# Kernel tuning notes

Hardware: AMD Instinct MI355X
Metric: run time of the kernel (lower is better)

The kernel has to match this reference:

```python
import jax, jax.numpy as jnp
import numpy as np

HEADS = 4
DIM_HEAD = 32
GROUPS = 32  # min(256//4, 32)
EPS = 1e-5


def setup_inputs() -> dict:
    key = jax.random.key(0)
    ks = jax.random.split(key, 5)
    B, C, H, W = 16, 256, 64, 64
    CD, HC, WC = 512, 32, 32
    hid = HEADS * DIM_HEAD  # 128
    return {
        "x": jax.random.normal(ks[0], (B, C, H, W), jnp.float32),
        "cond": jax.random.normal(ks[1], (B, CD, HC, WC), jnp.float32),
        "gn_w": jnp.ones((C,), jnp.float32),
        "gn_b": jnp.zeros((C,), jnp.float32),
        "w_q": jax.random.normal(ks[2], (hid, C), jnp.float32) * 0.05,
        "b_q": jnp.zeros((hid,), jnp.float32),
        "w_kv": jax.random.normal(ks[3], (2 * hid, CD), jnp.float32) * 0.05,
        "b_kv": jnp.zeros((2 * hid,), jnp.float32),
        "w_out": jax.random.normal(ks[4], (C, hid), jnp.float32) * 0.05,
        "b_out": jnp.zeros((C,), jnp.float32),
    }


def _group_norm(x, w, b):
    # x: (B, C, H, W); normalize per group over (channels-in-group, H, W)
    B, C, H, W = x.shape
    xg = x.reshape(B, GROUPS, C // GROUPS, H, W)
    mu = jnp.mean(xg, axis=(2, 3, 4), keepdims=True)
    var = jnp.var(xg, axis=(2, 3, 4), keepdims=True)
    xn = ((xg - mu) * jax.lax.rsqrt(var + EPS)).reshape(B, C, H, W)
    return xn * w[None, :, None, None] + b[None, :, None, None]


def _conv1x1(x, w, b):
    # x: (B, Cin, H, W), w: (Cout, Cin), b: (Cout,)
    return jnp.einsum('oc,bchw->bohw', w, x) + b[None, :, None, None]


def reference(x, cond, gn_w, gn_b, w_q, b_q, w_kv, b_kv, w_out, b_out):
    B, C, H, W = x.shape
    hid = HEADS * DIM_HEAD
    xn = _group_norm(x, gn_w, gn_b)
    q = _conv1x1(xn, w_q, b_q)          # (B, hid, H, W)
    kv = _conv1x1(cond, w_kv, b_kv)     # (B, 2*hid, Hc, Wc)
    Nc = kv.shape[2] * kv.shape[3]
    N = H * W
    k = kv[:, :hid].reshape(B, HEADS, DIM_HEAD, Nc)
    v = kv[:, hid:].reshape(B, HEADS, DIM_HEAD, Nc)
    q = q.reshape(B, HEADS, DIM_HEAD, N)
    k = jax.nn.softmax(k, axis=-1)
    # kv outer product: (B, heads, d, e)
    context = jnp.einsum('bhdn,bhen->bhde', k, v)
    # query contraction over d: (B, heads, e, n)
    out = jnp.einsum('bhde,bhdn->bhen', context, q)
    out = out.reshape(B, hid, H, W)
    return _conv1x1(out, w_out, b_out)
```

## Files before the change

kernel.cpp:

```cpp
#include <hip/hip_runtime.h>
#include <hip/hip_bf16.h>

typedef __attribute__((ext_vector_type(8))) short bf16x8;
typedef __attribute__((ext_vector_type(4))) float f32x4;

__device__ __forceinline__ ushort f2bf(float f) {
    __hip_bfloat16 h = __float2bfloat16(f);
    return __builtin_bit_cast(ushort, h);
}
__device__ __forceinline__ float bflo(unsigned u) { return __uint_as_float(u << 16); }
__device__ __forceinline__ float bfhi(unsigned u) { return __uint_as_float(u & 0xffff0000u); }

__device__ __forceinline__ void unpack8(uint4 r, float* o) {
    o[0] = bflo(r.x); o[1] = bfhi(r.x); o[2] = bflo(r.y); o[3] = bfhi(r.y);
    o[4] = bflo(r.z); o[5] = bfhi(r.z); o[6] = bflo(r.w); o[7] = bfhi(r.w);
}

__global__ void cvtw_kernel(const float* __restrict__ w, ushort* __restrict__ o,
                            float* __restrict__ zbase) {
    int i = blockIdx.x * 256 + threadIdx.x;
    if (i < 68608) zbase[i] = 0.f;
    o[i] = f2bf(w[i]);
}

__global__ __launch_bounds__(256) void kvstats_kernel(const ushort* __restrict__ wkv16,
                                                      const float* __restrict__ cond,
                                                      const float* __restrict__ b_kv,
                                                      ushort* __restrict__ kv16,
                                                      const float* __restrict__ x,
                                                      float* __restrict__ statacc) {
    __shared__ ushort lA[64 * 64];
    __shared__ ushort lB[64 * 64];
    __shared__ float scratch[64 * 64];
    __shared__ float red[8];
    int bid = blockIdx.x;
    int t = threadIdx.x;
    if (bid < 1024) {
        int nb = bid & 15, ob = (bid >> 4) & 3, b = bid >> 6;
        int col0 = nb * 64, row0 = ob * 64;
        int l = t & 63, wid = t >> 6;
        int wr = wid >> 1, wc = wid & 1;
        int lr = l & 15, lg = l >> 4;
        const ushort* Ab = wkv16 + (size_t)row0 * 512;
        const float* Bb = cond + (size_t)b * 512 * 1024 + col0;
        int sp = t & 31, sj = t >> 5;
        uint4 a0_, a1_;
        float4 b0_, b1_, b2_, b3_;
        int rA0 = t >> 3,        gA0 = (t & 7) ^ (rA0 & 7);
        int rA1 = 32 + (t >> 3), gA1 = (t & 7) ^ (rA1 & 7);
        int rB = t >> 4, gB = t & 15;
#define KV_LOADA(k0) { \
        a0_ = *(const uint4*)(Ab + (size_t)rA0 * 512 + (k0) + gA0 * 8); \
        a1_ = *(const uint4*)(Ab + (size_t)rA1 * 512 + (k0) + gA1 * 8); }
#define KV_LOADB(k0) { \
        b0_ = *(const float4*)&Bb[(size_t)((k0) + rB)      * 1024 + gB * 4]; \
        b1_ = *(const float4*)&Bb[(size_t)((k0) + 16 + rB) * 1024 + gB * 4]; \
        b2_ = *(const float4*)&Bb[(size_t)((k0) + 32 + rB) * 1024 + gB * 4]; \
        b3_ = *(const float4*)&Bb[(size_t)((k0) + 48 + rB) * 1024 + gB * 4]; }
        KV_LOADA(0); KV_LOADB(0);
        f32x4 acc00 = {}, acc01 = {}, acc10 = {}, acc11 = {};
        for (int it = 0; it < 8; ++it) {
            *(uint4*)((char*)lA + (size_t)t * 16) = a0_;
            *(uint4*)((char*)lA + (size_t)(256 + t) * 16) = a1_;
            *(float4*)((char*)scratch + (rB)      * 256 + (gB ^ (((rB)      >> 1) & 15)) * 16) = b0_;
            *(float4*)((char*)scratch + (16 + rB) * 256 + (gB ^ (((16 + rB) >> 1) & 15)) * 16) = b1_;
            *(float4*)((char*)scratch + (32 + rB) * 256 + (gB ^ (((32 + rB) >> 1) & 15)) * 16) = b2_;
            *(float4*)((char*)scratch + (48 + rB) * 256 + (gB ^ (((48 + rB) >> 1) & 15)) * 16) = b3_;
            __syncthreads();
            if (it < 7) { KV_LOADA(it * 64 + 64); KV_LOADB(it * 64 + 64); }
            {
                int swz = sp & 15;
                float4 s0 = *(const float4*)((char*)scratch + (2*sp)   * 256 + ((2*sj)   ^ swz) * 16);
                float4 s1 = *(const float4*)((char*)scratch + (2*sp)   * 256 + ((2*sj+1) ^ swz) * 16);
                float4 s2 = *(const float4*)((char*)scratch + (2*sp+1) * 256 + ((2*sj)   ^ swz) * 16);
                float4 s3 = *(const float4*)((char*)scratch + (2*sp+1) * 256 + ((2*sj+1) ^ swz) * 16);
                float c0v[8] = {s0.x, s0.y, s0.z, s0.w, s1.x, s1.y, s1.z, s1.w};
                float c1v[8] = {s2.x, s2.y, s2.z, s2.w, s3.x, s3.y, s3.z, s3.w};
                #pragma unroll
                for (int w = 0; w < 8; ++w) {
                    int n = sj * 8 + w;
                    unsigned pk = (unsigned)f2bf(c0v[w]) | ((unsigned)f2bf(c1v[w]) << 16);
                    *(unsigned*)((char*)lB + n * 128 + (((sp >> 2) ^ (n & 7)) * 16) + (sp & 3) * 4) = pk;
                }
            }
            __syncthreads();
            #pragma unroll
            for (int ks = 0; ks < 2; ++ks) {
                bf16x8 av0, av1, bv0, bv1;
                {
                    int ar = wr * 32 + lr, q = (ks * 4 + lg) ^ (ar & 7);
                    av0 = *(const bf16x8*)((const char*)lA + ar * 128 + q * 16);
                }
                {
                    int ar = wr * 32 + 16 + lr, q = (ks * 4 + lg) ^ (ar & 7);
                    av1 = *(const bf16x8*)((const char*)lA + ar * 128 + q * 16);
                }
                {
                    int br = wc * 32 + lr, q = (ks * 4 + lg) ^ (br & 7);
                    bv0 = *(const bf16x8*)((const char*)lB + br * 128 + q * 16);
                }
                {
                    int br = wc * 32 + 16 + lr, q = (ks * 4 + lg) ^ (br & 7);
                    bv1 = *(const bf16x8*)((const char*)lB + br * 128 + q * 16);
                }
                acc00 = __builtin_amdgcn_mfma_f32_16x16x32_bf16(av0, bv0, acc00, 0, 0, 0);
                acc01 = __builtin_amdgcn_mfma_f32_16x16x32_bf16(av0, bv1, acc01, 0, 0, 0);
                acc10 = __builtin_amdgcn_mfma_f32_16x16x32_bf16(av1, bv0, acc10, 0, 0, 0);
                acc11 = __builtin_amdgcn_mfma_f32_16x16x32_bf16(av1, bv1, acc11, 0, 0, 0);
            }
            __syncthreads();
        }
#undef KV_LOADA
#undef KV_LOADB
        int orow = row0 + wr * 32, ocol = col0 + wc * 32 + lr;
        #pragma unroll
        for (int mi = 0; mi < 2; ++mi) {
            int rb = orow + mi * 16 + lg * 4;
            float4 b4 = *(const float4*)&b_kv[rb];
            float bvr[4] = {b4.x, b4.y, b4.z, b4.w};
            f32x4 aacc0 = mi == 0 ? acc00 : acc10;
            f32x4 aacc1 = mi == 0 ? acc01 : acc11;
            #pragma unroll
            for (int r = 0; r < 4; ++r) {
                kv16[((size_t)b * 256 + rb + r) * 1024 + ocol]      = f2bf(aacc0[r] + bvr[r]);
                kv16[((size_t)b * 256 + rb + r) * 1024 + ocol + 16] = f2bf(aacc1[r] + bvr[r]);
            }
        }
    } else {
        int sid = bid - 1024;
        int bg = sid >> 2, q = sid & 3;
        const float4* xp = (const float4*)(x + (size_t)bg * 32768 + q * 8192);
        float s = 0.f, ss = 0.f;
        #pragma unroll
        for (int j = 0; j < 8; ++j) {
            float4 v = xp[t + 256 * j];
            s  += v.x + v.y + v.z + v.w;
            ss += v.x*v.x + v.y*v.y + v.z*v.z + v.w*v.w;
        }
        #pragma unroll
        for (int off = 32; off > 0; off >>= 1) {
            s  += __shfl_down(s, off, 64);
            ss += __shfl_down(ss, off, 64);
        }
        int wave = t >> 6;
        if ((t & 63) == 0) { red[wave * 2] = s; red[wave * 2 + 1] = ss; }
        __syncthreads();
        if (t == 0) {
            float S  = red[0] + red[2] + red[4] + red[6];
            float SS = red[1] + red[3] + red[5] + red[7];
            atomicAdd(&statacc[bg * 2],     S);
            atomicAdd(&statacc[bg * 2 + 1], SS);
        }
    }
}

__global__ __launch_bounds__(256) void ctx_partial_kernel(const ushort* __restrict__ kv,
                                                          float* __restrict__ rowsum,
                                                          float* __restrict__ ctx) {
    int bh = blockIdx.y, b = bh >> 2, h = bh & 3;
    int n0 = blockIdx.x * 128;
    __shared__ float pl[32][129], vl[32][129];
    int t = threadIdx.x;
    int r = t >> 3, cs = (t & 7) * 16;
    const ushort* kp = kv + ((size_t)b * 256 + h * 32 + r) * 1024 + n0 + cs;
    const ushort* vp = kv + ((size_t)b * 256 + 128 + h * 32 + r) * 1024 + n0 + cs;
    float kvals[16], vvals[16];
    unpack8(((const uint4*)kp)[0], kvals);
    unpack8(((const uint4*)kp)[1], kvals + 8);
    unpack8(((const uint4*)vp)[0], vvals);
    unpack8(((const uint4*)vp)[1], vvals + 8);
    float psum = 0.f;
    #pragma unroll
    for (int i = 0; i < 16; ++i) {
        float e = __expf(kvals[i]);
        pl[r][cs + i] = e;
        vl[r][cs + i] = vvals[i];
        psum += e;
    }
    psum += __shfl_xor(psum, 1, 64);
    psum += __shfl_xor(psum, 2, 64);
    psum += __shfl_xor(psum, 4, 64);
    if ((t & 7) == 0) atomicAdd(&rowsum[bh * 32 + r], psum);
    __syncthreads();
    int d0 = t >> 5, e0 = t & 31;
    float acc[4] = {0.f, 0.f, 0.f, 0.f};
    #pragma unroll 8
    for (int nn = 0; nn < 128; ++nn) {
        float vv = vl[e0][nn];
        #pragma unroll
        for (int i = 0; i < 4; ++i)
            acc[i] += pl[d0 + 8 * i][nn] * vv;
    }
    #pragma unroll
    for (int i = 0; i < 4; ++i)
        atomicAdd(&ctx[((size_t)bh * 32 + d0 + 8 * i) * 32 + e0], acc[i]);
}

__global__ __launch_bounds__(256) void a_kernel(const float* __restrict__ ctx,
                                                const float* __restrict__ rowsum,
                                                const float* __restrict__ w_out,
                                                const float* __restrict__ w_q,
                                                const float* __restrict__ b_q,
                                                const float* __restrict__ statacc,
                                                const float* __restrict__ gn_w,
                                                const float* __restrict__ gn_b,
                                                const float* __restrict__ b_out,
                                                ushort* __restrict__ A16,
                                                float* __restrict__ biasb) {
    __shared__ float ctxl[4][32][33];
    __shared__ float wol[16][128];
    __shared__ float ml[16][128];
    __shared__ float cbuf[256][17];
    __shared__ float pbuf[16][17];
    int b = blockIdx.x >> 4, ot = (blockIdx.x & 15) << 4;
    int t = threadIdx.x;
    #pragma unroll
    for (int j = 0; j < 16; ++j) {
        int e = t + 256 * j;
        float inv = 1.f / rowsum[b * 128 + (e >> 5)];
        ctxl[e >> 10][(e >> 5) & 31][e & 31] = ctx[(size_t)b * 4096 + e] * inv;
    }
    #pragma unroll
    for (int j = 0; j < 8; ++j) {
        int e = t + 256 * j;
        wol[e >> 7][e & 127] = w_out[(ot + (e >> 7)) * 128 + (e & 127)];
    }
    __syncthreads();
    #pragma unroll
    for (int j = 0; j < 8; ++j) {
        int e = t + 256 * j;
        int o = e >> 7, hd = e & 127, h = hd >> 5, d = hd & 31;
        float acc = 0.f;
        #pragma unroll
        for (int ee = 0; ee < 32; ++ee) acc += wol[o][h * 32 + ee] * ctxl[h][d][ee];
        ml[o][hd] = acc;
    }
    __syncthreads();
    int c = t, g = c >> 3;
    float a0 = statacc[(b * 32 + g) * 2], a1 = statacc[(b * 32 + g) * 2 + 1];
    float mu  = a0 * (1.f / 32768.f);
    float var = a1 * (1.f / 32768.f) - mu * mu;
    float sc = rsqrtf(var + 1e-5f) * gn_w[c];
    float tc = gn_b[c] - mu * sc;
    float wt[16];
    #pragma unroll
    for (int o = 0; o < 16; ++o) wt[o] = 0.f;
    for (int hd = 0; hd < 128; ++hd) {
        float wq = w_q[hd * 256 + c];
        #pragma unroll
        for (int o = 0; o < 16; ++o) wt[o] += ml[o][hd] * wq;
    }
    ushort* Abp = A16 + ((size_t)b * 256 + ot) * 256 + c;
    #pragma unroll
    for (int o = 0; o < 16; ++o) {
        Abp[(size_t)o * 256] = f2bf(wt[o] * sc);
        cbuf[c][o] = wt[o] * tc;
    }
    __syncthreads();
    {
        int o = t >> 4, seg = t & 15;
        float p = 0.f;
        #pragma unroll
        for (int i = 0; i < 16; ++i) p += cbuf[seg * 16 + i][o];
        pbuf[o][seg] = p;
    }
    __syncthreads();
    if (t < 16) {
        int o = t;
        float sum = 0.f;
        #pragma unroll
        for (int s2 = 0; s2 < 16; ++s2) sum += pbuf[o][s2];
        float md = 0.f;
        #pragma unroll 8
        for (int hd = 0; hd < 128; ++hd) md += ml[o][hd] * b_q[hd];
        biasb[(size_t)b * 256 + ot + o] = sum + md + b_out[ot + o];
    }
}

__global__ __launch_bounds__(512) void out_gemm_fused(const ushort* __restrict__ A16,
                                                      const float* __restrict__ x,
                                                      const float* __restrict__ biasb,
                                                      float* __restrict__ out) {
    __shared__ ushort lA[256 * 64];
    __shared__ ushort lB[128 * 64];
    __shared__ float scratch[64 * 128];
    int b = blockIdx.y;
    int n0 = blockIdx.x * 128;
    int t = threadIdx.x;
    int l = t & 63, wid = t >> 6;
    int wr = wid >> 1, wc = wid & 1;
    int lr = l & 15, lg = l >> 4;
    const ushort* Ab = A16 + (size_t)b * 65536;
    const float* xb = x + (size_t)b * 256 * 4096 + n0;
    int sp = t & 31, sj = t >> 5;
    uint4 a0_, a1_, a2_, a3_;
    float4 b0_, b1_, b2_, b3_;
    int rA = t >> 3, gA = (t & 7) ^ (rA & 7);
    int rB = t >> 5, gB = t & 31;
#define OG_LOADA(k0) { \
    a0_ = *(const uint4*)(Ab + (size_t)(rA)       * 256 + (k0) + gA * 8); \
    a1_ = *(const uint4*)(Ab + (size_t)(64 + rA)  * 256 + (k0) + gA * 8); \
    a2_ = *(const uint4*)(Ab + (size_t)(128 + rA) * 256 + (k0) + gA * 8); \
    a3_ = *(const uint4*)(Ab + (size_t)(192 + rA) * 256 + (k0) + gA * 8); }
#define OG_LOADB(k0) { \
    b0_ = *(const float4*)&xb[(size_t)((k0) + rB)      * 4096 + gB * 4]; \
    b1_ = *(const float4*)&xb[(size_t)((k0) + 16 + rB) * 4096 + gB * 4]; \
    b2_ = *(const float4*)&xb[(size_t)((k0) + 32 + rB) * 4096 + gB * 4]; \
    b3_ = *(const float4*)&xb[(size_t)((k0) + 48 + rB) * 4096 + gB * 4]; }
    OG_LOADA(0); OG_LOADB(0);
    f32x4 acc[4][4] = {};
    for (int it = 0; it < 4; ++it) {
        *(uint4*)((char*)lA + (size_t)t * 16)          = a0_;
        *(uint4*)((char*)lA + (size_t)(512 + t) * 16)  = a1_;
        *(uint4*)((char*)lA + (size_t)(1024 + t) * 16) = a2_;
        *(uint4*)((char*)lA + (size_t)(1536 + t) * 16) = a3_;
        *(float4*)((char*)scratch + (rB)      * 512 + (gB ^ (((rB)      >> 1) & 31)) * 16) = b0_;
        *(float4*)((char*)scratch + (16 + rB) * 512 + (gB ^ (((16 + rB) >> 1) & 31)) * 16) = b1_;
        *(float4*)((char*)scratch + (32 + rB) * 512 + (gB ^ (((32 + rB) >> 1) & 31)) * 16) = b2_;
        *(float4*)((char*)scratch + (48 + rB) * 512 + (gB ^ (((48 + rB) >> 1) & 31)) * 16) = b3_;
        __syncthreads();
        if (it < 3) { OG_LOADA(it * 64 + 64); OG_LOADB(it * 64 + 64); }
        {
            int swz = sp & 31;
            float4 s0 = *(const float4*)((char*)scratch + (2*sp)   * 512 + ((2*sj)   ^ swz) * 16);
            float4 s1 = *(const float4*)((char*)scratch + (2*sp)   * 512 + ((2*sj+1) ^ swz) * 16);
            float4 s2 = *(const float4*)((char*)scratch + (2*sp+1) * 512 + ((2*sj)   ^ swz) * 16);
            float4 s3 = *(const float4*)((char*)scratch + (2*sp+1) * 512 + ((2*sj+1) ^ swz) * 16);
            float c0v[8] = {s0.x, s0.y, s0.z, s0.w, s1.x, s1.y, s1.z, s1.w};
            float c1v[8] = {s2.x, s2.y, s2.z, s2.w, s3.x, s3.y, s3.z, s3.w};
            #pragma unroll
            for (int w = 0; w < 8; ++w) {
                int n = sj * 8 + w;
                unsigned pk = (unsigned)f2bf(c0v[w]) | ((unsigned)f2bf(c1v[w]) << 16);
                *(unsigned*)((char*)lB + n * 128 + (((sp >> 2) ^ (n & 7)) * 16) + (sp & 3) * 4) = pk;
            }
        }
        __syncthreads();
        #pragma unroll
        for (int ks = 0; ks < 2; ++ks) {
            bf16x8 av[4], bv[4];
            #pragma unroll
            for (int mi = 0; mi < 4; ++mi) {
                int ar = wr * 64 + mi * 16 + lr;
                int q = (ks * 4 + lg) ^ (ar & 7);
                av[mi] = *(const bf16x8*)((const char*)lA + ar * 128 + q * 16);
            }
            #pragma unroll
            for (int ni = 0; ni < 4; ++ni) {
                int br = wc * 64 + ni * 16 + lr;
                int q = (ks * 4 + lg) ^ (br & 7);
                bv[ni] = *(const bf16x8*)((const char*)lB + br * 128 + q * 16);
            }
            #pragma unroll
            for (int mi = 0; mi < 4; ++mi)
                #pragma unroll
                for (int ni = 0; ni < 4; ++ni)
                    acc[mi][ni] = __builtin_amdgcn_mfma_f32_16x16x32_bf16(
                        av[mi], bv[ni], acc[mi][ni], 0, 0, 0);
        }
        __syncthreads();
    }
#undef OG_LOADA
#undef OG_LOADB
    const float* bp = biasb + (size_t)b * 256;
    int orow = wr * 64, ocol = n0 + wc * 64 + lr;
    #pragma unroll
    for (int mi = 0; mi < 4; ++mi) {
        int rb = orow + mi * 16 + lg * 4;
        float4 b4 = *(const float4*)&bp[rb];
        float bvr[4] = {b4.x, b4.y, b4.z, b4.w};
        #pragma unroll
        for (int ni = 0; ni < 4; ++ni) {
            int cc = ocol + ni * 16;
            #pragma unroll
            for (int r = 0; r < 4; ++r)
                out[((size_t)b * 256 + rb + r) * 4096 + cc] = acc[mi][ni][r] + bvr[r];
        }
    }
}

extern "C" void kernel_launch(void* const* d_in, const int* in_sizes, int n_in,
                              void* d_out, int out_size, void* d_ws, size_t ws_size,
                              hipStream_t stream) {
    const float* x     = (const float*)d_in[0];
    const float* cond  = (const float*)d_in[1];
    const float* gn_w  = (const float*)d_in[2];
    const float* gn_b  = (const float*)d_in[3];
    const float* w_q   = (const float*)d_in[4];
    const float* b_q   = (const float*)d_in[5];
    const float* w_kv  = (const float*)d_in[6];
    const float* b_kv  = (const float*)d_in[7];
    const float* w_out = (const float*)d_in[8];
    const float* b_out = (const float*)d_in[9];
    float* out = (float*)d_out;

    float* f       = (float*)d_ws;
    float* statacc = f;
    float* rowsum  = f + 1024;
    float* ctx     = f + 3072;
    float* biasb   = f + 68608;
    ushort* u      = (ushort*)(f + 72704);
    ushort* wkv16  = u;
    ushort* kv16   = u + 131072;
    ushort* A16    = u + 4325376;

    cvtw_kernel<<<512, 256, 0, stream>>>(w_kv, wkv16, statacc);
    kvstats_kernel<<<3072, 256, 0, stream>>>(wkv16, cond, b_kv, kv16, x, statacc);
    ctx_partial_kernel<<<dim3(8, 64), 256, 0, stream>>>(kv16, rowsum, ctx);
    a_kernel<<<256, 256, 0, stream>>>(ctx, rowsum, w_out, w_q, b_q, statacc,
                                      gn_w, gn_b, b_out, A16, biasb);
    out_gemm_fused<<<dim3(32, 16), 512, 0, stream>>>(A16, x, biasb, out);
}
```

Baseline: 85.92 us.

## Split KV GEMM from stats, enlarge GEMM tile, move stats into prep kernel

The group-norm statistics pass moves out of the combined KV/stats kernel and into the weight-conversion kernel. Each block now reduces a whole group and writes the result directly, so the atomics are gone and statacc no longer needs zeroing. The KV GEMM becomes its own kernel with a 128x64 output tile, four 16x16 MFMA tiles per wave along M, and a two-stage register prefetch of the cond tiles, which halves redundant cond reads across output-row blocks. The cost is fewer GEMM blocks (512 instead of 1024), higher register pressure, and the loss of overlap between the stats reduction and the GEMM inside one launch.

```diff
diff --git a/kernel.cpp b/kernel.cpp
--- a/kernel.cpp
+++ b/kernel.cpp
@@ -16,123 +16,23 @@
     o[4] = bflo(r.z); o[5] = bfhi(r.z); o[6] = bflo(r.w); o[7] = bfhi(r.w);
 }
 
-__global__ void cvtw_kernel(const float* __restrict__ w, ushort* __restrict__ o,
-                            float* __restrict__ zbase) {
-    int i = blockIdx.x * 256 + threadIdx.x;
-    if (i < 68608) zbase[i] = 0.f;
-    o[i] = f2bf(w[i]);
-}
-
-__global__ __launch_bounds__(256) void kvstats_kernel(const ushort* __restrict__ wkv16,
-                                                      const float* __restrict__ cond,
-                                                      const float* __restrict__ b_kv,
-                                                      ushort* __restrict__ kv16,
-                                                      const float* __restrict__ x,
-                                                      float* __restrict__ statacc) {
-    __shared__ ushort lA[64 * 64];
-    __shared__ ushort lB[64 * 64];
-    __shared__ float scratch[64 * 64];
+__global__ __launch_bounds__(256) void prep_kernel(const float* __restrict__ w,
+                                                   ushort* __restrict__ o,
+                                                   float* __restrict__ zbase,
+                                                   const float* __restrict__ x,
+                                                   float* __restrict__ statacc) {
     __shared__ float red[8];
-    int bid = blockIdx.x;
-    int t = threadIdx.x;
-    if (bid < 1024) {
-        int nb = bid & 15, ob = (bid >> 4) & 3, b = bid >> 6;
-        int col0 = nb * 64, row0 = ob * 64;
-        int l = t & 63, wid = t >> 6;
-        int wr = wid >> 1, wc = wid & 1;
-        int lr = l & 15, lg = l >> 4;
-        const ushort* Ab = wkv16 + (size_t)row0 * 512;
-        const float* Bb = cond + (size_t)b * 512 * 1024 + col0;
-        int sp = t & 31, sj = t >> 5;
-        uint4 a0_, a1_;
-        float4 b0_, b1_, b2_, b3_;
-        int rA0 = t >> 3,        gA0 = (t & 7) ^ (rA0 & 7);
-        int rA1 = 32 + (t >> 3), gA1 = (t & 7) ^ (rA1 & 7);
-        int rB = t >> 4, gB = t & 15;
-#define KV_LOADA(k0) { \
-        a0_ = *(const uint4*)(Ab + (size_t)rA0 * 512 + (k0) + gA0 * 8); \
-        a1_ = *(const uint4*)(Ab + (size_t)rA1 * 512 + (k0) + gA1 * 8); }
-#define KV_LOADB(k0) { \
-        b0_ = *(const float4*)&Bb[(size_t)((k0) + rB)      * 1024 + gB * 4]; \
-        b1_ = *(const float4*)&Bb[(size_t)((k0) + 16 + rB) * 1024 + gB * 4]; \
-        b2_ = *(const float4*)&Bb[(size_t)((k0) + 32 + rB) * 1024 + gB * 4]; \
-        b3_ = *(const float4*)&Bb[(size_t)((k0) + 48 + rB) * 1024 + gB * 4]; }
-        KV_LOADA(0); KV_LOADB(0);
-        f32x4 acc00 = {}, acc01 = {}, acc10 = {}, acc11 = {};
-        for (int it = 0; it < 8; ++it) {
-            *(uint4*)((char*)lA + (size_t)t * 16) = a0_;
-            *(uint4*)((char*)lA + (size_t)(256 + t) * 16) = a1_;
-            *(float4*)((char*)scratch + (rB)      * 256 + (gB ^ (((rB)      >> 1) & 15)) * 16) = b0_;
-            *(float4*)((char*)scratch + (16 + rB) * 256 + (gB ^ (((16 + rB) >> 1) & 15)) * 16) = b1_;
-            *(float4*)((char*)scratch + (32 + rB) * 256 + (gB ^ (((32 + rB) >> 1) & 15)) * 16) = b2_;
-            *(float4*)((char*)scratch + (48 + rB) * 256 + (gB ^ (((48 + rB) >> 1) & 15)) * 16) = b3_;
-            __syncthreads();
-            if (it < 7) { KV_LOADA(it * 64 + 64); KV_LOADB(it * 64 + 64); }
-            {
-                int swz = sp & 15;
-                float4 s0 = *(const float4*)((char*)scratch + (2*sp)   * 256 + ((2*sj)   ^ swz) * 16);
-                float4 s1 = *(const float4*)((char*)scratch + (2*sp)   * 256 + ((2*sj+1) ^ swz) * 16);
-                float4 s2 = *(const float4*)((char*)scratch + (2*sp+1) * 256 + ((2*sj)   ^ swz) * 16);
-                float4 s3 = *(const float4*)((char*)scratch + (2*sp+1) * 256 + ((2*sj+1) ^ swz) * 16);
-                float c0v[8] = {s0.x, s0.y, s0.z, s0.w, s1.x, s1.y, s1.z, s1.w};
-                float c1v[8] = {s2.x, s2.y, s2.z, s2.w, s3.x, s3.y, s3.z, s3.w};
-                #pragma unroll
-                for (int w = 0; w < 8; ++w) {
-                    int n = sj * 8 + w;
-                    unsigned pk = (unsigned)f2bf(c0v[w]) | ((unsigned)f2bf(c1v[w]) << 16);
-                    *(unsigned*)((char*)lB + n * 128 + (((sp >> 2) ^ (n & 7)) * 16) + (sp & 3) * 4) = pk;
-                }
-            }
-            __syncthreads();
-            #pragma unroll
-            for (int ks = 0; ks < 2; ++ks) {
-                bf16x8 av0, av1, bv0, bv1;
-                {
-                    int ar = wr * 32 + lr, q = (ks * 4 + lg) ^ (ar & 7);
-                    av0 = *(const bf16x8*)((const char*)lA + ar * 128 + q * 16);
-                }
-                {
-                    int ar = wr * 32 + 16 + lr, q = (ks * 4 + lg) ^ (ar & 7);
-                    av1 = *(const bf16x8*)((const char*)lA + ar * 128 + q * 16);
-                }
-                {
-                    int br = wc * 32 + lr, q = (ks * 4 + lg) ^ (br & 7);
-                    bv0 = *(const bf16x8*)((const char*)lB + br * 128 + q * 16);
-                }
-                {
-                    int br = wc * 32 + 16 + lr, q = (ks * 4 + lg) ^ (br & 7);
-                    bv1 = *(const bf16x8*)((const char*)lB + br * 128 + q * 16);
-                }
-                acc00 = __builtin_amdgcn_mfma_f32_16x16x32_bf16(av0, bv0, acc00, 0, 0, 0);
-                acc01 = __builtin_amdgcn_mfma_f32_16x16x32_bf16(av0, bv1, acc01, 0, 0, 0);
-                acc10 = __builtin_amdgcn_mfma_f32_16x16x32_bf16(av1, bv0, acc10, 0, 0, 0);
-                acc11 = __builtin_amdgcn_mfma_f32_16x16x32_bf16(av1, bv1, acc11, 0, 0, 0);
-            }
-            __syncthreads();
-        }
-#undef KV_LOADA
-#undef KV_LOADB
-        int orow = row0 + wr * 32, ocol = col0 + wc * 32 + lr;
-        #pragma unroll
-        for (int mi = 0; mi < 2; ++mi) {
-            int rb = orow + mi * 16 + lg * 4;
-            float4 b4 = *(const float4*)&b_kv[rb];
-            float bvr[4] = {b4.x, b4.y, b4.z, b4.w};
-            f32x4 aacc0 = mi == 0 ? acc00 : acc10;
-            f32x4 aacc1 = mi == 0 ? acc01 : acc11;
-            #pragma unroll
-            for (int r = 0; r < 4; ++r) {
-                kv16[((size_t)b * 256 + rb + r) * 1024 + ocol]      = f2bf(aacc0[r] + bvr[r]);
-                kv16[((size_t)b * 256 + rb + r) * 1024 + ocol + 16] = f2bf(aacc1[r] + bvr[r]);
-            }
-        }
+    int bid = blockIdx.x, t = threadIdx.x;
+    if (bid < 512) {
+        int i = bid * 256 + t;
+        if (i < 67584) zbase[i] = 0.f;
+        o[i] = f2bf(w[i]);
     } else {
-        int sid = bid - 1024;
-        int bg = sid >> 2, q = sid & 3;
-        const float4* xp = (const float4*)(x + (size_t)bg * 32768 + q * 8192);
+        int bg = bid - 512;
+        const float4* xp = (const float4*)(x + (size_t)bg * 32768);
         float s = 0.f, ss = 0.f;
         #pragma unroll
-        for (int j = 0; j < 8; ++j) {
+        for (int j = 0; j < 32; ++j) {
             float4 v = xp[t + 256 * j];
             s  += v.x + v.y + v.z + v.w;
             ss += v.x*v.x + v.y*v.y + v.z*v.z + v.w*v.w;
@@ -146,10 +46,138 @@
         if ((t & 63) == 0) { red[wave * 2] = s; red[wave * 2 + 1] = ss; }
         __syncthreads();
         if (t == 0) {
-            float S  = red[0] + red[2] + red[4] + red[6];
-            float SS = red[1] + red[3] + red[5] + red[7];
-            atomicAdd(&statacc[bg * 2],     S);
-            atomicAdd(&statacc[bg * 2 + 1], SS);
+            statacc[bg * 2]     = red[0] + red[2] + red[4] + red[6];
+            statacc[bg * 2 + 1] = red[1] + red[3] + red[5] + red[7];
+        }
+    }
+}
+
+__global__ __launch_bounds__(256) void kv_gemm(const ushort* __restrict__ wkv16,
+                                               const float* __restrict__ cond,
+                                               const float* __restrict__ b_kv,
+                                               ushort* __restrict__ kv16) {
+    __shared__ ushort lA[128 * 64];
+    __shared__ ushort lB[64 * 64];
+    __shared__ float scratch[64 * 64];
+    int nb = blockIdx.x, ob = blockIdx.y, b = blockIdx.z;
+    int col0 = nb * 64, row0 = ob * 128;
+    int t = threadIdx.x;
+    int l = t & 63, wid = t >> 6;
+    int wr = wid >> 1, wc = wid & 1;
+    int lr = l & 15, lg = l >> 4;
+    const ushort* Ab = wkv16 + (size_t)row0 * 512;
+    const float* Bb = cond + (size_t)b * 512 * 1024 + col0;
+    int sp = t & 31, sj = t >> 5;
+    int rA_ = t >> 3;
+    int gA_ = (t & 7) ^ (rA_ & 7);
+    int rB = t >> 4, gB = t & 15;
+    uint4 a0_, a1_, a2_, a3_;
+    float4 b0_, b1_, b2_, b3_;
+    float4 c0_, c1_, c2_, c3_;
+#define KG_LOADA(k0) { \
+    a0_ = *(const uint4*)(Ab + (size_t)(rA_)      * 512 + (k0) + gA_ * 8); \
+    a1_ = *(const uint4*)(Ab + (size_t)(32 + rA_) * 512 + (k0) + gA_ * 8); \
+    a2_ = *(const uint4*)(Ab + (size_t)(64 + rA_) * 512 + (k0) + gA_ * 8); \
+    a3_ = *(const uint4*)(Ab + (size_t)(96 + rA_) * 512 + (k0) + gA_ * 8); }
+#define KG_LOADB0(k0) { \
+    b0_ = *(const float4*)&Bb[(size_t)((k0) + rB)      * 1024 + gB * 4]; \
+    b1_ = *(const float4*)&Bb[(size_t)((k0) + 16 + rB) * 1024 + gB * 4]; \
+    b2_ = *(const float4*)&Bb[(size_t)((k0) + 32 + rB) * 1024 + gB * 4]; \
+    b3_ = *(const float4*)&Bb[(size_t)((k0) + 48 + rB) * 1024 + gB * 4]; }
+#define KG_LOADB1(k0) { \
+    c0_ = *(const float4*)&Bb[(size_t)((k0) + rB)      * 1024 + gB * 4]; \
+    c1_ = *(const float4*)&Bb[(size_t)((k0) + 16 + rB) * 1024 + gB * 4]; \
+    c2_ = *(const float4*)&Bb[(size_t)((k0) + 32 + rB) * 1024 + gB * 4]; \
+    c3_ = *(const float4*)&Bb[(size_t)((k0) + 48 + rB) * 1024 + gB * 4]; }
+#define KG_WRITEA() { \
+    *(uint4*)((char*)lA + (size_t)(t) * 16)       = a0_; \
+    *(uint4*)((char*)lA + (size_t)(256 + t) * 16) = a1_; \
+    *(uint4*)((char*)lA + (size_t)(512 + t) * 16) = a2_; \
+    *(uint4*)((char*)lA + (size_t)(768 + t) * 16) = a3_; }
+#define KG_WRITEB(v0, v1, v2, v3) { \
+    *(float4*)((char*)scratch + (rB)      * 256 + (gB ^ (((rB)      >> 1) & 15)) * 16) = v0; \
+    *(float4*)((char*)scratch + (16 + rB) * 256 + (gB ^ (((16 + rB) >> 1) & 15)) * 16) = v1; \
+    *(float4*)((char*)scratch + (32 + rB) * 256 + (gB ^ (((32 + rB) >> 1) & 15)) * 16) = v2; \
+    *(float4*)((char*)scratch + (48 + rB) * 256 + (gB ^ (((48 + rB) >> 1) & 15)) * 16) = v3; }
+#define KG_PACK() { \
+    int swz = sp & 15; \
+    float4 s0 = *(const float4*)((char*)scratch + (2*sp)   * 256 + ((2*sj)   ^ swz) * 16); \
+    float4 s1 = *(const float4*)((char*)scratch + (2*sp)   * 256 + ((2*sj+1) ^ swz) * 16); \
+    float4 s2 = *(const float4*)((char*)scratch + (2*sp+1) * 256 + ((2*sj)   ^ swz) * 16); \
+    float4 s3 = *(const float4*)((char*)scratch + (2*sp+1) * 256 + ((2*sj+1) ^ swz) * 16); \
+    float c0v[8] = {s0.x, s0.y, s0.z, s0.w, s1.x, s1.y, s1.z, s1.w}; \
+    float c1v[8] = {s2.x, s2.y, s2.z, s2.w, s3.x, s3.y, s3.z, s3.w}; \
+    _Pragma("unroll") \
+    for (int w = 0; w < 8; ++w) { \
+        int n = sj * 8 + w; \
+        unsigned pk = (unsigned)f2bf(c0v[w]) | ((unsigned)f2bf(c1v[w]) << 16); \
+        *(unsigned*)((char*)lB + n * 128 + (((sp >> 2) ^ (n & 7)) * 16) + (sp & 3) * 4) = pk; \
+    } }
+#define KG_MFMA() { \
+    _Pragma("unroll") \
+    for (int ks = 0; ks < 2; ++ks) { \
+        bf16x8 av[4], bv[2]; \
+        _Pragma("unroll") \
+        for (int mi = 0; mi < 4; ++mi) { \
+            int ar = wr * 64 + mi * 16 + lr; \
+            int q = (ks * 4 + lg) ^ (ar & 7); \
+            av[mi] = *(const bf16x8*)((const char*)lA + ar * 128 + q * 16); \
+        } \
+        _Pragma("unroll") \
+        for (int ni = 0; ni < 2; ++ni) { \
+            int br = wc * 32 + ni * 16 + lr; \
+            int q = (ks * 4 + lg) ^ (br & 7); \
+            bv[ni] = *(const bf16x8*)((const char*)lB + br * 128 + q * 16); \
+        } \
+        _Pragma("unroll") \
+        for (int mi = 0; mi < 4; ++mi) \
+            _Pragma("unroll") \
+            for (int ni = 0; ni < 2; ++ni) \
+                acc[mi][ni] = __builtin_amdgcn_mfma_f32_16x16x32_bf16( \
+                    av[mi], bv[ni], acc[mi][ni], 0, 0, 0); \
+    } }
+    KG_LOADA(0); KG_LOADB0(0); KG_LOADB1(64);
+    f32x4 acc[4][2] = {};
+    #pragma unroll
+    for (int ii = 0; ii < 4; ++ii) {
+        int k0 = ii * 128;
+        KG_WRITEA();
+        KG_WRITEB(b0_, b1_, b2_, b3_);
+        __syncthreads();
+        KG_LOADA(k0 + 64);
+        if (ii < 3) KG_LOADB0(k0 + 128);
+        KG_PACK();
+        __syncthreads();
+        KG_MFMA();
+        __syncthreads();
+        KG_WRITEA();
+        KG_WRITEB(c0_, c1_, c2_, c3_);
+        __syncthreads();
+        if (ii < 3) { KG_LOADA(k0 + 128); KG_LOADB1(k0 + 192); }
+        KG_PACK();
+        __syncthreads();
+        KG_MFMA();
+        __syncthreads();
+    }
+#undef KG_LOADA
+#undef KG_LOADB0
+#undef KG_LOADB1
+#undef KG_WRITEA
+#undef KG_WRITEB
+#undef KG_PACK
+#undef KG_MFMA
+    int orow = row0 + wr * 64, ocol = col0 + wc * 32 + lr;
+    #pragma unroll
+    for (int mi = 0; mi < 4; ++mi) {
+        int rb = orow + mi * 16 + lg * 4;
+        float4 b4 = *(const float4*)&b_kv[rb];
+        float bvr[4] = {b4.x, b4.y, b4.z, b4.w};
+        #pragma unroll
+        for (int ni = 0; ni < 2; ++ni) {
+            int cc = ocol + ni * 16;
+            #pragma unroll
+            for (int r = 0; r < 4; ++r)
+                kv16[((size_t)b * 256 + rb + r) * 1024 + cc] = f2bf(acc[mi][ni][r] + bvr[r]);
         }
     }
 }
@@ -404,8 +432,8 @@
     ushort* kv16   = u + 131072;
     ushort* A16    = u + 4325376;
 
-    cvtw_kernel<<<512, 256, 0, stream>>>(w_kv, wkv16, statacc);
-    kvstats_kernel<<<3072, 256, 0, stream>>>(wkv16, cond, b_kv, kv16, x, statacc);
+    prep_kernel<<<1024, 256, 0, stream>>>(w_kv, wkv16, rowsum, x, statacc);
+    kv_gemm<<<dim3(16, 2, 16), 256, 0, stream>>>(wkv16, cond, b_kv, kv16);
     ctx_partial_kernel<<<dim3(8, 64), 256, 0, stream>>>(kv16, rowsum, ctx);
     a_kernel<<<256, 256, 0, stream>>>(ctx, rowsum, w_out, w_q, b_q, statacc,
                                       gn_w, gn_b, b_out, A16, biasb);
```

Result: faster. 84.10 us (-2.1%).
